# Kernel tuning notes

Hardware: AMD Instinct MI355X
Metric: run time of the kernel (lower is better)

Reference implementation:

```python
import jax, jax.numpy as jnp
import numpy as np

N, E, M = 4096, 65536, 16   # nodes, edges, channel multiplicity per degree
MID = 32                    # RadialFunc hidden width (SE3-Transformer default)
EPS = 1e-5                  # BatchNorm1d eps
DEGS = [0, 1]
PAIRS = [(0, 0), (0, 1), (1, 0), (1, 1)]  # (d_in, d_out)


def _bn_relu(x, g, b):
    # BatchNorm1d in training mode (biased batch stats over edges) + ReLU
    mu = x.mean(0, keepdims=True)
    var = ((x - mu) ** 2).mean(0, keepdims=True)
    return jax.nn.relu((x - mu) / jnp.sqrt(var + EPS) * g + b)


def _radial(feat, w1, b1, g1, be1, w2, b2, g2, be2, w3, b3, nf):
    # RadialFunc: Linear-BN-ReLU, Linear-BN-ReLU, Linear -> [E, nc_out, 1, nc_in, 1, nf]
    y = _bn_relu(feat @ w1 + b1, g1, be1)
    y = _bn_relu(y @ w2 + b2, g2, be2)
    y = y @ w3 + b3
    return y.reshape(-1, M, 1, M, 1, nf)


def _forward(h0, h1, r, basis00, basis01, basis10, basis11,
             rw1, rb1, rg1, rbe1, rw2, rb2, rg2, rbe2,
             w3_00, b3_00, w3_01, b3_01, w3_10, b3_10, w3_11, b3_11,
             Wself0, Wself1, edge_src, edge_dst):
    h = {0: h0, 1: h1}
    basis = {(0, 0): basis00, (0, 1): basis01, (1, 0): basis10, (1, 1): basis11}
    w3b3 = {(0, 0): (w3_00, b3_00), (0, 1): (w3_01, b3_01),
            (1, 0): (w3_10, b3_10), (1, 1): (w3_11, b3_11)}
    Wself = {0: Wself0, 1: Wself1}
    # PairwiseConv: per-edge kernel = sum_f R * basis  -> [E, M, 2do+1, M, 2di+1]
    kern = {}
    for p, (di, do) in enumerate(PAIRS):
        nf = 2 * min(di, do) + 1
        w3, b3 = w3b3[(di, do)]
        R = _radial(r, rw1[p], rb1[p], rg1[p], rbe1[p],
                    rw2[p], rb2[p], rg2[p], rbe2[p], w3, b3, nf)
        kern[(di, do)] = (R * basis[(di, do)]).sum(-1)
    cnt = jnp.maximum(
        jax.ops.segment_sum(jnp.ones((E,), h0.dtype), edge_dst, num_segments=N), 1.0)
    outs = []
    for do in DEGS:
        msg = jnp.zeros((E, M, 2 * do + 1), h0.dtype)
        for di in DEGS:
            # per-edge small matmul: kernel @ gathered source feature
            msg = msg + jnp.einsum('eopiq,eiq->eop', kern[(di, do)], h[di][edge_src])
        # self-interaction, flavor='skip': add W @ destination feature per edge
        msg = msg + jnp.einsum('mi,eip->emp', Wself[do][0], h[do][edge_dst])
        s = jax.ops.segment_sum(msg, edge_dst, num_segments=N)  # scatter-mean
        outs.append(s / cnt[:, None, None])
    return tuple(outs)


def setup_inputs() -> dict:
    key = jax.random.key(0)
    ks = jax.random.split(key, 20)
    nrm = lambda k, sh, s=1.0: jax.random.normal(k, sh, jnp.float32) * s
    return {
        'h0': nrm(ks[0], (N, M, 1)),
        'h1': nrm(ks[1], (N, M, 3)),
        'r': jax.random.uniform(ks[2], (E, 1), jnp.float32),
        'basis00': nrm(ks[3], (E, 1, 1, 1, 1, 1)),
        'basis01': nrm(ks[4], (E, 1, 3, 1, 1, 1)),
        'basis10': nrm(ks[5], (E, 1, 1, 1, 3, 1)),
        'basis11': nrm(ks[6], (E, 1, 3, 1, 3, 3)),
        'rw1': nrm(ks[7], (4, 1, MID)),
        'rb1': jnp.zeros((4, MID), jnp.float32),
        'rg1': jnp.ones((4, MID), jnp.float32),
        'rbe1': jnp.zeros((4, MID), jnp.float32),
        'rw2': nrm(ks[8], (4, MID, MID), 1.0 / np.sqrt(MID)),
        'rb2': jnp.zeros((4, MID), jnp.float32),
        'rg2': jnp.ones((4, MID), jnp.float32),
        'rbe2': jnp.zeros((4, MID), jnp.float32),
        'w3_00': nrm(ks[9], (MID, M * M), 1.0 / np.sqrt(MID)),
        'b3_00': jnp.zeros((M * M,), jnp.float32),
        'w3_01': nrm(ks[10], (MID, M * M), 1.0 / np.sqrt(MID)),
        'b3_01': jnp.zeros((M * M,), jnp.float32),
        'w3_10': nrm(ks[11], (MID, M * M), 1.0 / np.sqrt(MID)),
        'b3_10': jnp.zeros((M * M,), jnp.float32),
        'w3_11': nrm(ks[12], (MID, M * M * 3), 1.0 / np.sqrt(MID)),
        'b3_11': jnp.zeros((M * M * 3,), jnp.float32),
        'Wself0': nrm(ks[13], (1, M, M), 1.0 / np.sqrt(M)),
        'Wself1': nrm(ks[14], (1, M, M), 1.0 / np.sqrt(M)),
        'edge_src': jax.random.randint(ks[15], (E,), 0, N),
        'edge_dst': jax.random.randint(ks[16], (E,), 0, N),
    }


def reference(h0, h1, r, basis00, basis01, basis10, basis11,
              rw1, rb1, rg1, rbe1, rw2, rb2, rg2, rbe2,
              w3_00, b3_00, w3_01, b3_01, w3_10, b3_10, w3_11, b3_11,
              Wself0, Wself1, edge_src, edge_dst):
    return _forward(h0, h1, r, basis00, basis01, basis10, basis11,
                    rw1, rb1, rg1, rbe1, rw2, rb2, rg2, rbe2,
                    w3_00, b3_00, w3_01, b3_01, w3_10, b3_10, w3_11, b3_11,
                    Wself0, Wself1, edge_src, edge_dst)
```

## Files before the change

kernel.cpp:

```cpp
#include <hip/hip_runtime.h>

#define N_NODES 4096
#define N_EDGES 65536
#define MID 32
#define BN_EPS 1e-5f

#define WS_RSUM    0
#define WS_RSUMSQ  1
#define WS_ALPHA1  272
#define WS_BETA1   400
#define WS_A2      528
#define WS_S2      656
#define WS_W2T     16384
#define WS_GRAM    20480
#define WS_SUMY    24576
#define WS_MSG_F   262144
#define WS_U00     4456448
#define WS_U01     4521984
#define WS_V10     4587520
#define WS_W11     4784128
#define WS_DEG_I   1024
#define WS_CUR_I   5120
#define WS_OFFS_I  9216
#define WS_ELIST_I 65536
#define WSB_WA     524288
#define WSB_WB     557056
#define WSB_WC     573440

typedef short bf16x8 __attribute__((ext_vector_type(8)));
typedef float f32x4  __attribute__((ext_vector_type(4)));

__device__ __forceinline__ unsigned short f2bf(float x) {
    unsigned u = __float_as_uint(x);
    u += 0x7fffu + ((u >> 16) & 1u);
    return (unsigned short)(u >> 16);
}

__global__ void __launch_bounds__(256) k_pre(const float* __restrict__ rw2,
        const float* __restrict__ w300, const float* __restrict__ w301,
        const float* __restrict__ w310, const float* __restrict__ w311,
        const float* __restrict__ bw300, const float* __restrict__ bw301,
        const float* __restrict__ bw310, const float* __restrict__ bw311,
        const float* __restrict__ r, const int* __restrict__ edst,
        const float* __restrict__ h0, const float* __restrict__ h1,
        float* __restrict__ wsf) {
    if (blockIdx.x < 128) {
        int t = blockIdx.x * 256 + threadIdx.x;
        char* wsb = (char*)wsf;
        if (t < 4096) {
            int p = t >> 10, rem = t & 1023, c = rem >> 5, k = rem & 31;
            wsf[WS_W2T + t] = rw2[(p << 10) + (k << 5) + c];
        }
        if (t < 16384) {
            int col = t >> 5, k = t & 31;
            float v = (col < 256) ? w300[(k << 8) + col] : w310[(k << 8) + (col - 256)];
            ((unsigned short*)(wsb + WSB_WA))[t] = f2bf(v);
        }
        if (t < 8192) {
            int col = t >> 5, k = t & 31;
            ((unsigned short*)(wsb + WSB_WB))[t] = f2bf(w301[(k << 8) + col]);
        }
        if (t < 24576) {
            int col = t >> 5, k = t & 31;
            int f = col >> 8, rem = col & 255;
            ((unsigned short*)(wsb + WSB_WC))[t] = f2bf(w311[k * 768 + rem * 3 + f]);
        }
    } else if (blockIdx.x < 384) {
        int e = (blockIdx.x - 128) * 256 + threadIdx.x;
        float v = r[e];
        atomicAdd(((int*)wsf) + WS_DEG_I + edst[e], 1);
        float s = v, ss = v * v;
#pragma unroll
        for (int mk = 32; mk >= 1; mk >>= 1) {
            s  += __shfl_xor(s,  mk, 64);
            ss += __shfl_xor(ss, mk, 64);
        }
        __shared__ float ls[4], lss[4];
        int lane = threadIdx.x & 63, wv = threadIdx.x >> 6;
        if (lane == 0) { ls[wv] = s; lss[wv] = ss; }
        __syncthreads();
        if (threadIdx.x == 0) {
            atomicAdd(wsf + WS_RSUM,   ls[0] + ls[1] + ls[2] + ls[3]);
            atomicAdd(wsf + WS_RSUMSQ, lss[0] + lss[1] + lss[2] + lss[3]);
        }
    } else {
        int g = (blockIdx.x - 384) * 256 + threadIdx.x;
        int n = g >> 4, mo = g & 15;
        float s00 = 0.f, s01 = 0.f;
#pragma unroll
        for (int mi = 0; mi < 16; ++mi) {
            float hv = h0[n * 16 + mi];
            s00 += bw300[mo * 16 + mi] * hv;
            s01 += bw301[mo * 16 + mi] * hv;
        }
        wsf[WS_U00 + n * 16 + mo] = s00;
        wsf[WS_U01 + n * 16 + mo] = s01;
#pragma unroll
        for (int q = 0; q < 3; ++q) {
            float sv = 0.f;
#pragma unroll
            for (int mi = 0; mi < 16; ++mi)
                sv += bw310[mo * 16 + mi] * h1[n * 48 + mi * 3 + q];
            wsf[WS_V10 + n * 48 + q * 16 + mo] = sv;
        }
#pragma unroll 1
        for (int f = 0; f < 3; ++f)
#pragma unroll 1
            for (int q = 0; q < 3; ++q) {
                float sv = 0.f;
#pragma unroll
                for (int mi = 0; mi < 16; ++mi)
                    sv += bw311[(mo * 16 + mi) * 3 + f] * h1[n * 48 + mi * 3 + q];
                wsf[WS_W11 + n * 144 + (f * 3 + q) * 16 + mo] = sv;
            }
    }
}

__global__ void __launch_bounds__(512) k_gram(const float* __restrict__ r,
        const float* __restrict__ rw1, const float* __restrict__ rg1,
        const float* __restrict__ rbe1, float* __restrict__ wsf) {
    int t = threadIdx.x;
    int wv = t >> 6, lane = t & 63;
    int quad = lane >> 4, lq = lane & 15;
    int p  = __builtin_amdgcn_readfirstlane(wv & 3);
    int mt = __builtin_amdgcn_readfirstlane(wv >> 2);
    float mu_r  = wsf[WS_RSUM] * (1.f / N_EDGES);
    float var_r = wsf[WS_RSUMSQ] * (1.f / N_EDGES) - mu_r * mu_r;
    float al[2], be[2];
#pragma unroll
    for (int hh = 0; hh < 2; ++hh) {
        int ch = p * 32 + hh * 16 + lq;
        float w1 = rw1[ch];
        float a = w1 * rg1[ch] * rsqrtf(w1 * w1 * var_r + BN_EPS);
        al[hh] = a;
        be[hh] = rbe1[ch] - a * mu_r;
    }
    bf16x8 ones;
#pragma unroll
    for (int j = 0; j < 8; ++j) ones[j] = (short)0x3F80;
    f32x4 accG0 = {0.f, 0.f, 0.f, 0.f};
    f32x4 accG1 = {0.f, 0.f, 0.f, 0.f};
    f32x4 accS  = {0.f, 0.f, 0.f, 0.f};
    int ebase = blockIdx.x * 1024;
#pragma unroll 1
    for (int ks = 0; ks < 32; ++ks) {
        const float* rp = r + ebase + ks * 32 + quad * 8;
        float4 ra = *(const float4*)(rp);
        float4 rb = *(const float4*)(rp + 4);
        float rv[8] = {ra.x, ra.y, ra.z, ra.w, rb.x, rb.y, rb.z, rb.w};
        bf16x8 fr0, fr1;
#pragma unroll
        for (int j = 0; j < 8; ++j) {
            fr0[j] = (short)f2bf(fmaxf(0.f, al[0] * rv[j] + be[0]));
            fr1[j] = (short)f2bf(fmaxf(0.f, al[1] * rv[j] + be[1]));
        }
        bf16x8 fA = mt ? fr1 : fr0;
        accG0 = __builtin_amdgcn_mfma_f32_16x16x32_bf16(fA, fr0, accG0, 0, 0, 0);
        accG1 = __builtin_amdgcn_mfma_f32_16x16x32_bf16(fA, fr1, accG1, 0, 0, 0);
        accS  = __builtin_amdgcn_mfma_f32_16x16x32_bf16(fA, ones, accS,  0, 0, 0);
    }
    float* G = wsf + WS_GRAM + p * 1024;
#pragma unroll
    for (int reg = 0; reg < 4; ++reg) {
        int k1 = mt * 16 + quad * 4 + reg;
        atomicAdd(&G[k1 * 32 + lq],      accG0[reg]);
        atomicAdd(&G[k1 * 32 + 16 + lq], accG1[reg]);
    }
    if (lq == 0) {
#pragma unroll
        for (int reg = 0; reg < 4; ++reg)
            atomicAdd(wsf + WS_SUMY + p * 32 + mt * 16 + quad * 4 + reg, accS[reg]);
    }
}

__global__ void __launch_bounds__(1024) k_fs(const float* __restrict__ rw1,
        const float* __restrict__ rg1, const float* __restrict__ rbe1,
        const float* __restrict__ rg2, const float* __restrict__ rbe2,
        const float* __restrict__ rb2, float* __restrict__ wsf) {
    int t = threadIdx.x;
    if (t < 128) {
        float mu_r  = wsf[WS_RSUM] * (1.f / N_EDGES);
        float var_r = wsf[WS_RSUMSQ] * (1.f / N_EDGES) - mu_r * mu_r;
        float w1 = rw1[t];
        float al = w1 * rg1[t] * rsqrtf(w1 * w1 * var_r + BN_EPS);
        wsf[WS_ALPHA1 + t] = al;
        wsf[WS_BETA1  + t] = rbe1[t] - al * mu_r;
        int p = t >> 5, c = t & 31;
        const float* G = wsf + WS_GRAM + p * 1024;
        const float* w = wsf + WS_W2T + p * 1024 + c * 32;
        float invE = 1.f / N_EDGES;
        float s1 = 0.f;
#pragma unroll 1
        for (int k = 0; k < 32; ++k) s1 += w[k] * (wsf[WS_SUMY + p * 32 + k] * invE);
        float q = 0.f;
#pragma unroll 1
        for (int k1 = 0; k1 < 32; ++k1) {
            float a = 0.f;
#pragma unroll
            for (int k2 = 0; k2 < 32; ++k2) a += w[k2] * G[k1 * 32 + k2];
            q += w[k1] * a;
        }
        float var = q * invE - s1 * s1;
        float a2 = rg2[t] * rsqrtf(var + BN_EPS);
        wsf[WS_A2 + t] = a2;
        float mu2 = rb2[t] + s1;
        wsf[WS_S2 + t] = rbe2[t] - mu2 * a2;
    }
    __shared__ int sdata[1024];
    const int* deg = ((const int*)wsf) + WS_DEG_I;
    int* offs = ((int*)wsf) + WS_OFFS_I;
    int* cur  = ((int*)wsf) + WS_CUR_I;
    int v0 = deg[t * 4], v1 = deg[t * 4 + 1], v2 = deg[t * 4 + 2], v3 = deg[t * 4 + 3];
    sdata[t] = v0 + v1 + v2 + v3;
    __syncthreads();
    for (int off = 1; off < 1024; off <<= 1) {
        int x = sdata[t];
        int y = (t >= off) ? sdata[t - off] : 0;
        __syncthreads();
        sdata[t] = x + y;
        __syncthreads();
    }
    int excl = (t == 0) ? 0 : sdata[t - 1];
    int o0 = excl, o1 = excl + v0, o2 = o1 + v1, o3 = o2 + v2;
    offs[t * 4] = o0;     cur[t * 4] = o0;
    offs[t * 4 + 1] = o1; cur[t * 4 + 1] = o1;
    offs[t * 4 + 2] = o2; cur[t * 4 + 2] = o2;
    offs[t * 4 + 3] = o3; cur[t * 4 + 3] = o3;
    if (t == 1023) offs[4096] = sdata[1023];
}

__global__ void k_bucket(const int* __restrict__ edst, float* __restrict__ wsf) {
    int e = blockIdx.x * 256 + threadIdx.x;
    int d = edst[e];
    int* cur   = ((int*)wsf) + WS_CUR_I;
    int* elist = ((int*)wsf) + WS_ELIST_I;
    int pos = atomicAdd(&cur[d], 1);
    elist[pos] = e;
}

__global__ void __launch_bounds__(256) k_corr(const float* __restrict__ b00,
        const float* __restrict__ b01, const float* __restrict__ b10,
        const float* __restrict__ b11, const int* __restrict__ esrc,
        const float* __restrict__ wsf, float* __restrict__ msg) {
    int g = blockIdx.x * 256 + threadIdx.x;
    int e = g >> 2, quad = g & 3;
    int s = esrc[e];
    float4 u00q = *(const float4*)(wsf + WS_U00 + s * 16 + quad * 4);
    float b00v = b00[e];
    float m0[4];
#pragma unroll
    for (int rr = 0; rr < 4; ++rr) m0[rr] = b00v * ((const float*)&u00q)[rr];
#pragma unroll
    for (int q = 0; q < 3; ++q) {
        float4 vq = *(const float4*)(wsf + WS_V10 + s * 48 + q * 16 + quad * 4);
        float bq = b10[e * 3 + q];
#pragma unroll
        for (int rr = 0; rr < 4; ++rr) m0[rr] += bq * ((const float*)&vq)[rr];
    }
    {
        float4 w = {m0[0], m0[1], m0[2], m0[3]};
        *(float4*)(msg + (size_t)e * 64 + quad * 4) = w;
    }
    float4 u01q = *(const float4*)(wsf + WS_U01 + s * 16 + quad * 4);
    float bo0 = b01[e * 3 + 0], bo1 = b01[e * 3 + 1], bo2 = b01[e * 3 + 2];
    float m1[4][3];
#pragma unroll
    for (int rr = 0; rr < 4; ++rr) {
        float u = ((const float*)&u01q)[rr];
        m1[rr][0] = bo0 * u; m1[rr][1] = bo1 * u; m1[rr][2] = bo2 * u;
    }
#pragma unroll
    for (int f = 0; f < 3; ++f)
#pragma unroll
        for (int q = 0; q < 3; ++q) {
            float4 wq = *(const float4*)(wsf + WS_W11 + s * 144 + (f * 3 + q) * 16 + quad * 4);
#pragma unroll
            for (int o = 0; o < 3; ++o) {
                float bas = b11[e * 27 + o * 9 + q * 3 + f];
#pragma unroll
                for (int rr = 0; rr < 4; ++rr) m1[rr][o] += bas * ((const float*)&wq)[rr];
            }
        }
    float* base = msg + (size_t)e * 64 + 16 + quad * 12;
    float4 w0 = {m1[0][0], m1[0][1], m1[0][2], m1[1][0]};
    float4 w1 = {m1[1][1], m1[1][2], m1[2][0], m1[2][1]};
    float4 w2 = {m1[2][2], m1[3][0], m1[3][1], m1[3][2]};
    *(float4*)(base)     = w0;
    *(float4*)(base + 4) = w1;
    *(float4*)(base + 8) = w2;
}

__device__ __forceinline__ void y2_lds16(int p, int el, int c0, float rv,
                                         const float* __restrict__ wsf,
                                         const float* __restrict__ rb2, char* dst) {
    float y1[MID];
#pragma unroll
    for (int k = 0; k < MID; ++k)
        y1[k] = fmaxf(0.f, wsf[WS_ALPHA1 + p * 32 + k] * rv + wsf[WS_BETA1 + p * 32 + k]);
    unsigned short h[16];
#pragma unroll
    for (int cc = 0; cc < 16; ++cc) {
        int c = c0 + cc;
        float x = rb2[p * 32 + c];
#pragma unroll
        for (int k = 0; k < MID; ++k) x += y1[k] * wsf[WS_W2T + p * 1024 + c * 32 + k];
        h[cc] = f2bf(fmaxf(0.f, wsf[WS_A2 + p * 32 + c] * x + wsf[WS_S2 + p * 32 + c]));
    }
#pragma unroll
    for (int q = 0; q < 2; ++q) {
        int4 pk;
        pk.x = (int)h[q * 8 + 0] | ((int)h[q * 8 + 1] << 16);
        pk.y = (int)h[q * 8 + 2] | ((int)h[q * 8 + 3] << 16);
        pk.z = (int)h[q * 8 + 4] | ((int)h[q * 8 + 5] << 16);
        pk.w = (int)h[q * 8 + 6] | ((int)h[q * 8 + 7] << 16);
        *(int4*)(dst + el * 64 + c0 * 2 + q * 16) = pk;
    }
}

__global__ void __launch_bounds__(512, 2) k_msg(const float* __restrict__ r,
        const float* __restrict__ h0, const float* __restrict__ h1,
        const float* __restrict__ b00, const float* __restrict__ b01,
        const float* __restrict__ b10, const float* __restrict__ b11,
        const float* __restrict__ rb2,
        const int* __restrict__ esrc,
        const float* __restrict__ wsf, float* __restrict__ msg) {
    extern __shared__ char smem[];
    short* w3s = (short*)smem;
    const char* wsb = (const char*)wsf;
    int t = threadIdx.x;
    int wv = t >> 6, lane = t & 63;
    int quad = lane >> 4, lq = lane & 15;
    int eb = blockIdx.x << 8;

    {
        const float4* src = (const float4*)(wsb + WSB_WA);
        float4* dst = (float4*)smem;
#pragma unroll
        for (int i = 0; i < 4; ++i) dst[i * 512 + t] = src[i * 512 + t];
    }
    {
        int p = __builtin_amdgcn_readfirstlane((t >> 8) * 2);
        int el = t & 255;
        float rv = r[eb + el];
        char* dst = smem + 32768 + (t >> 8) * 16384;
        y2_lds16(p, el, 0, rv, wsf, rb2, dst);
        y2_lds16(p, el, 16, rv, wsf, rb2, dst);
    }
    __syncthreads();
#pragma unroll
    for (int g2 = 0; g2 < 2; ++g2) {
        int el = (wv * 2 + g2) * 16 + lq;
        int e = eb + el;
        int s = esrc[e];
        bf16x8 bf0 = *(const bf16x8*)(smem + 32768 + el * 64 + quad * 16);
        bf16x8 bf2 = *(const bf16x8*)(smem + 49152 + el * 64 + quad * 16);
        float4 h0q = *(const float4*)(h0 + s * 16 + quad * 4);
        float4 hv0 = *(const float4*)(h1 + s * 48 + quad * 12);
        float4 hv1 = *(const float4*)(h1 + s * 48 + quad * 12 + 4);
        float4 hv2 = *(const float4*)(h1 + s * 48 + quad * 12 + 8);
        float b00v = b00[e];
        float bq0 = b10[e * 3 + 0], bq1 = b10[e * 3 + 1], bq2 = b10[e * 3 + 2];
        float gq0 = bq0 * hv0.x + bq1 * hv0.y + bq2 * hv0.z;
        float gq1 = bq0 * hv0.w + bq1 * hv1.x + bq2 * hv1.y;
        float gq2 = bq0 * hv1.z + bq1 * hv1.w + bq2 * hv2.x;
        float gq3 = bq0 * hv2.y + bq1 * hv2.z + bq2 * hv2.w;
        float4 a0v = *(const float4*)(msg + (size_t)e * 64 + quad * 4);
        float a0[4] = {a0v.x, a0v.y, a0v.z, a0v.w};
#pragma unroll
        for (int m = 0; m < 16; ++m) {
            bf16x8 af = *(const bf16x8*)(w3s + (m * 16 + lq) * 32 + quad * 8);
            f32x4 dd = __builtin_amdgcn_mfma_f32_16x16x32_bf16(af, bf0, (f32x4){0.f,0.f,0.f,0.f}, 0, 0, 0);
            float partial = dd[0] * h0q.x + dd[1] * h0q.y + dd[2] * h0q.z + dd[3] * h0q.w;
            partial += __shfl_xor(partial, 16);
            partial += __shfl_xor(partial, 32);
            a0[m & 3] += (quad == (m >> 2)) ? b00v * partial : 0.f;
        }
#pragma unroll
        for (int m = 0; m < 16; ++m) {
            bf16x8 af = *(const bf16x8*)(w3s + ((256 + m * 16 + lq) << 5) + quad * 8);
            f32x4 dd = __builtin_amdgcn_mfma_f32_16x16x32_bf16(af, bf2, (f32x4){0.f,0.f,0.f,0.f}, 0, 0, 0);
            float partial = dd[0] * gq0 + dd[1] * gq1 + dd[2] * gq2 + dd[3] * gq3;
            partial += __shfl_xor(partial, 16);
            partial += __shfl_xor(partial, 32);
            a0[m & 3] += (quad == (m >> 2)) ? partial : 0.f;
        }
        float4 w = {a0[0], a0[1], a0[2], a0[3]};
        *(float4*)(msg + (size_t)e * 64 + quad * 4) = w;
    }
    __syncthreads();

    {
        const float4* src = (const float4*)(wsb + WSB_WB);
        float4* dst = (float4*)smem;
#pragma unroll
        for (int i = 0; i < 2; ++i) dst[i * 512 + t] = src[i * 512 + t];
    }
    {
        int el = t & 255, c0 = (t >> 8) * 16;
        y2_lds16(1, el, c0, r[eb + el], wsf, rb2, smem + 16384);
    }
    __syncthreads();
#pragma unroll
    for (int g2 = 0; g2 < 2; ++g2) {
        int el = (wv * 2 + g2) * 16 + lq;
        int e = eb + el;
        int s = esrc[e];
        bf16x8 bf1 = *(const bf16x8*)(smem + 16384 + el * 64 + quad * 16);
        float4 h0q = *(const float4*)(h0 + s * 16 + quad * 4);
        float d1[4] = {0.f, 0.f, 0.f, 0.f};
#pragma unroll
        for (int m = 0; m < 16; ++m) {
            bf16x8 af = *(const bf16x8*)(w3s + (m * 16 + lq) * 32 + quad * 8);
            f32x4 dd = __builtin_amdgcn_mfma_f32_16x16x32_bf16(af, bf1, (f32x4){0.f,0.f,0.f,0.f}, 0, 0, 0);
            float partial = dd[0] * h0q.x + dd[1] * h0q.y + dd[2] * h0q.z + dd[3] * h0q.w;
            partial += __shfl_xor(partial, 16);
            partial += __shfl_xor(partial, 32);
            d1[m & 3] += (quad == (m >> 2)) ? partial : 0.f;
        }
        float bo0 = b01[e * 3 + 0], bo1 = b01[e * 3 + 1], bo2 = b01[e * 3 + 2];
        float* base = msg + (size_t)e * 64 + 16 + quad * 12;
        float4 r0 = *(const float4*)(base);
        float4 r1 = *(const float4*)(base + 4);
        float4 r2 = *(const float4*)(base + 8);
        float4 w0 = {r0.x + bo0 * d1[0], r0.y + bo1 * d1[0], r0.z + bo2 * d1[0], r0.w + bo0 * d1[1]};
        float4 w1 = {r1.x + bo1 * d1[1], r1.y + bo2 * d1[1], r1.z + bo0 * d1[2], r1.w + bo1 * d1[2]};
        float4 w2 = {r2.x + bo2 * d1[2], r2.y + bo0 * d1[3], r2.z + bo1 * d1[3], r2.w + bo2 * d1[3]};
        *(float4*)(base)     = w0;
        *(float4*)(base + 4) = w1;
        *(float4*)(base + 8) = w2;
    }
    __syncthreads();

    {
        const float4* src = (const float4*)(wsb + WSB_WC);
        float4* dst = (float4*)smem;
#pragma unroll
        for (int i = 0; i < 6; ++i) dst[i * 512 + t] = src[i * 512 + t];
    }
    {
        int el = t & 255, c0 = (t >> 8) * 16;
        y2_lds16(3, el, c0, r[eb + el], wsf, rb2, smem + 49152);
    }
    __syncthreads();
#pragma unroll
    for (int g2 = 0; g2 < 2; ++g2) {
        int el = (wv * 2 + g2) * 16 + lq;
        int e = eb + el;
        int s = esrc[e];
        bf16x8 bf3 = *(const bf16x8*)(smem + 49152 + el * 64 + quad * 16);
        float4 hv0 = *(const float4*)(h1 + s * 48 + quad * 12);
        float4 hv1 = *(const float4*)(h1 + s * 48 + quad * 12 + 4);
        float4 hv2 = *(const float4*)(h1 + s * 48 + quad * 12 + 8);
        float h1v[4][3] = {{hv0.x, hv0.y, hv0.z}, {hv0.w, hv1.x, hv1.y},
                           {hv1.z, hv1.w, hv2.x}, {hv2.y, hv2.z, hv2.w}};
        float m1[4][3];
#pragma unroll
        for (int rr = 0; rr < 4; ++rr)
#pragma unroll
            for (int o = 0; o < 3; ++o) m1[rr][o] = 0.f;
#pragma unroll
        for (int f = 0; f < 3; ++f) {
            float Tf[4][3];
#pragma unroll
            for (int o = 0; o < 3; ++o) {
                float bv0 = b11[e * 27 + o * 9 + 0 + f];
                float bv1 = b11[e * 27 + o * 9 + 3 + f];
                float bv2 = b11[e * 27 + o * 9 + 6 + f];
#pragma unroll
                for (int rr = 0; rr < 4; ++rr)
                    Tf[rr][o] = h1v[rr][0] * bv0 + h1v[rr][1] * bv1 + h1v[rr][2] * bv2;
            }
#pragma unroll
            for (int m = 0; m < 16; ++m) {
                int colb = f * 256 + m * 16 + lq;
                bf16x8 af = *(const bf16x8*)(w3s + colb * 32 + quad * 8);
                f32x4 dd = __builtin_amdgcn_mfma_f32_16x16x32_bf16(af, bf3, (f32x4){0.f,0.f,0.f,0.f}, 0, 0, 0);
#pragma unroll
                for (int o = 0; o < 3; ++o) {
                    float po = dd[0] * Tf[0][o] + dd[1] * Tf[1][o] + dd[2] * Tf[2][o] + dd[3] * Tf[3][o];
                    po += __shfl_xor(po, 16);
                    po += __shfl_xor(po, 32);
                    m1[m & 3][o] += (quad == (m >> 2)) ? po : 0.f;
                }
            }
        }
        float* base = msg + (size_t)e * 64 + 16 + quad * 12;
        float4 r0 = *(const float4*)(base);
        float4 r1 = *(const float4*)(base + 4);
        float4 r2 = *(const float4*)(base + 8);
        float4 w0 = {m1[0][0] + r0.x, m1[0][1] + r0.y, m1[0][2] + r0.z, m1[1][0] + r0.w};
        float4 w1 = {m1[1][1] + r1.x, m1[1][2] + r1.y, m1[2][0] + r1.z, m1[2][1] + r1.w};
        float4 w2 = {m1[2][2] + r2.x, m1[3][0] + r2.y, m1[3][1] + r2.z, m1[3][2] + r2.w};
        *(float4*)(base)     = w0;
        *(float4*)(base + 4) = w1;
        *(float4*)(base + 8) = w2;
    }
}

__global__ void __launch_bounds__(256) k_gather(const float* __restrict__ h0,
        const float* __restrict__ h1, const float* __restrict__ Wself0,
        const float* __restrict__ Wself1, const float* __restrict__ wsf,
        float* __restrict__ out) {
    int wv = threadIdx.x >> 6, lane = threadIdx.x & 63;
    int n = blockIdx.x * 4 + wv;
    const int* offs  = ((const int*)wsf) + WS_OFFS_I;
    const int* elist = ((const int*)wsf) + WS_ELIST_I;
    const float* msg = wsf + WS_MSG_F;
    int start = offs[n], end = offs[n + 1];
    int deg = end - start;
    float acc = 0.f;
    for (int j0 = 0; j0 < deg; j0 += 64) {
        int cnt = min(64, deg - j0);
        int eidv = (j0 + lane < deg) ? elist[start + j0 + lane] : 0;
        for (int jj = 0; jj < cnt; ++jj) {
            int eid = __shfl(eidv, jj);
            acc += msg[(size_t)eid * 64 + lane];
        }
    }
    float self = 0.f;
    if (lane < 16) {
        int m = lane;
#pragma unroll
        for (int i = 0; i < 16; ++i) self += Wself0[m * 16 + i] * h0[n * 16 + i];
    } else {
        int idx = lane - 16; int m = idx / 3, o = idx % 3;
#pragma unroll
        for (int i = 0; i < 16; ++i) self += Wself1[m * 16 + i] * h1[n * 48 + i * 3 + o];
    }
    float c = (float)(deg > 0 ? deg : 1);
    float res = acc / c + (deg > 0 ? self : 0.f);
    if (lane < 16) out[n * 16 + lane] = res;
    else           out[65536 + n * 48 + (lane - 16)] = res;
}

extern "C" void kernel_launch(void* const* d_in, const int* in_sizes, int n_in,
                              void* d_out, int out_size, void* d_ws, size_t ws_size,
                              hipStream_t stream) {
    const float* h0   = (const float*)d_in[0];
    const float* h1   = (const float*)d_in[1];
    const float* r    = (const float*)d_in[2];
    const float* b00  = (const float*)d_in[3];
    const float* b01  = (const float*)d_in[4];
    const float* b10  = (const float*)d_in[5];
    const float* b11  = (const float*)d_in[6];
    const float* rw1  = (const float*)d_in[7];
    const float* rg1  = (const float*)d_in[9];
    const float* rbe1 = (const float*)d_in[10];
    const float* rw2  = (const float*)d_in[11];
    const float* rb2  = (const float*)d_in[12];
    const float* rg2  = (const float*)d_in[13];
    const float* rbe2 = (const float*)d_in[14];
    const float* w300 = (const float*)d_in[15];
    const float* bw300= (const float*)d_in[16];
    const float* w301 = (const float*)d_in[17];
    const float* bw301= (const float*)d_in[18];
    const float* w310 = (const float*)d_in[19];
    const float* bw310= (const float*)d_in[20];
    const float* w311 = (const float*)d_in[21];
    const float* bw311= (const float*)d_in[22];
    const float* Wself0 = (const float*)d_in[23];
    const float* Wself1 = (const float*)d_in[24];
    const int* esrc = (const int*)d_in[25];
    const int* edst = (const int*)d_in[26];
    float* out = (float*)d_out;
    float* wsf = (float*)d_ws;
    float* msg = wsf + WS_MSG_F;

    static bool attr_set = false;
    if (!attr_set) {
        hipFuncSetAttribute((const void*)k_msg,
                            hipFuncAttributeMaxDynamicSharedMemorySize, 65536);
        attr_set = true;
    }

    hipMemsetAsync(d_ws, 0, 20480, stream);
    hipMemsetAsync((char*)d_ws + 81920, 0, 16896, stream);

    k_pre<<<640, 256, 0, stream>>>(rw2, w300, w301, w310, w311,
                                   bw300, bw301, bw310, bw311, r, edst, h0, h1, wsf);
    k_gram<<<64, 512, 0, stream>>>(r, rw1, rg1, rbe1, wsf);
    k_fs<<<1, 1024, 0, stream>>>(rw1, rg1, rbe1, rg2, rbe2, rb2, wsf);
    k_bucket<<<256, 256, 0, stream>>>(edst, wsf);
    k_corr<<<1024, 256, 0, stream>>>(b00, b01, b10, b11, esrc, wsf, msg);
    k_msg<<<256, 512, 65536, stream>>>(r, h0, h1, b00, b01, b10, b11, rb2,
                                       esrc, wsf, msg);
    k_gather<<<1024, 256, 0, stream>>>(h0, h1, Wself0, Wself1, wsf, out);
}
```

Measured before the change: 265.7 us.

## Fuse bias-correction pass into message kernel, halve edges per block, unroll gather

Removes the separate k_corr kernel and computes its U00/V10/U01/W11 correction terms directly inside k_msg, so the message buffer is no longer written and then read back for every edge. k_msg now handles 128 edges per block over 512 blocks with smaller shared memory, and each wave processes one 16-edge group instead of two. k_gram is split across twice as many blocks, the workspace is rearranged so a single memset covers it, and the gather loop is unrolled by four to keep more loads in flight. The trade-off is more per-thread arithmetic in k_msg and half the threads sitting idle during some y2 staging phases.

New measurement: 307.9 us. 15.9% more time.

```diff
diff --git a/kernel.cpp b/kernel.cpp
--- a/kernel.cpp
+++ b/kernel.cpp
@@ -11,17 +11,17 @@
 #define WS_BETA1   400
 #define WS_A2      528
 #define WS_S2      656
-#define WS_W2T     16384
-#define WS_GRAM    20480
-#define WS_SUMY    24576
+#define WS_GRAM    5120
+#define WS_SUMY    9216
+#define WS_W2T     17664
 #define WS_MSG_F   262144
 #define WS_U00     4456448
 #define WS_U01     4521984
 #define WS_V10     4587520
 #define WS_W11     4784128
 #define WS_DEG_I   1024
-#define WS_CUR_I   5120
-#define WS_OFFS_I  9216
+#define WS_CUR_I   9344
+#define WS_OFFS_I  13440
 #define WS_ELIST_I 65536
 #define WSB_WA     524288
 #define WSB_WB     557056
@@ -141,9 +141,9 @@
     f32x4 accG0 = {0.f, 0.f, 0.f, 0.f};
     f32x4 accG1 = {0.f, 0.f, 0.f, 0.f};
     f32x4 accS  = {0.f, 0.f, 0.f, 0.f};
-    int ebase = blockIdx.x * 1024;
+    int ebase = blockIdx.x * 512;
 #pragma unroll 1
-    for (int ks = 0; ks < 32; ++ks) {
+    for (int ks = 0; ks < 16; ++ks) {
         const float* rp = r + ebase + ks * 32 + quad * 8;
         float4 ra = *(const float4*)(rp);
         float4 rb = *(const float4*)(rp + 4);
@@ -238,58 +238,6 @@
     elist[pos] = e;
 }
 
-__global__ void __launch_bounds__(256) k_corr(const float* __restrict__ b00,
-        const float* __restrict__ b01, const float* __restrict__ b10,
-        const float* __restrict__ b11, const int* __restrict__ esrc,
-        const float* __restrict__ wsf, float* __restrict__ msg) {
-    int g = blockIdx.x * 256 + threadIdx.x;
-    int e = g >> 2, quad = g & 3;
-    int s = esrc[e];
-    float4 u00q = *(const float4*)(wsf + WS_U00 + s * 16 + quad * 4);
-    float b00v = b00[e];
-    float m0[4];
-#pragma unroll
-    for (int rr = 0; rr < 4; ++rr) m0[rr] = b00v * ((const float*)&u00q)[rr];
-#pragma unroll
-    for (int q = 0; q < 3; ++q) {
-        float4 vq = *(const float4*)(wsf + WS_V10 + s * 48 + q * 16 + quad * 4);
-        float bq = b10[e * 3 + q];
-#pragma unroll
-        for (int rr = 0; rr < 4; ++rr) m0[rr] += bq * ((const float*)&vq)[rr];
-    }
-    {
-        float4 w = {m0[0], m0[1], m0[2], m0[3]};
-        *(float4*)(msg + (size_t)e * 64 + quad * 4) = w;
-    }
-    float4 u01q = *(const float4*)(wsf + WS_U01 + s * 16 + quad * 4);
-    float bo0 = b01[e * 3 + 0], bo1 = b01[e * 3 + 1], bo2 = b01[e * 3 + 2];
-    float m1[4][3];
-#pragma unroll
-    for (int rr = 0; rr < 4; ++rr) {
-        float u = ((const float*)&u01q)[rr];
-        m1[rr][0] = bo0 * u; m1[rr][1] = bo1 * u; m1[rr][2] = bo2 * u;
-    }
-#pragma unroll
-    for (int f = 0; f < 3; ++f)
-#pragma unroll
-        for (int q = 0; q < 3; ++q) {
-            float4 wq = *(const float4*)(wsf + WS_W11 + s * 144 + (f * 3 + q) * 16 + quad * 4);
-#pragma unroll
-            for (int o = 0; o < 3; ++o) {
-                float bas = b11[e * 27 + o * 9 + q * 3 + f];
-#pragma unroll
-                for (int rr = 0; rr < 4; ++rr) m1[rr][o] += bas * ((const float*)&wq)[rr];
-            }
-        }
-    float* base = msg + (size_t)e * 64 + 16 + quad * 12;
-    float4 w0 = {m1[0][0], m1[0][1], m1[0][2], m1[1][0]};
-    float4 w1 = {m1[1][1], m1[1][2], m1[2][0], m1[2][1]};
-    float4 w2 = {m1[2][2], m1[3][0], m1[3][1], m1[3][2]};
-    *(float4*)(base)     = w0;
-    *(float4*)(base + 4) = w1;
-    *(float4*)(base + 8) = w2;
-}
-
 __device__ __forceinline__ void y2_lds16(int p, int el, int c0, float rv,
                                          const float* __restrict__ wsf,
                                          const float* __restrict__ rb2, char* dst) {
@@ -330,7 +278,9 @@
     int t = threadIdx.x;
     int wv = t >> 6, lane = t & 63;
     int quad = lane >> 4, lq = lane & 15;
-    int eb = blockIdx.x << 8;
+    int eb = blockIdx.x << 7;
+    int el = wv * 16 + lq;
+    int e = eb + el;
 
     {
         const float4* src = (const float4*)(wsb + WSB_WA);
@@ -339,21 +289,17 @@
         for (int i = 0; i < 4; ++i) dst[i * 512 + t] = src[i * 512 + t];
     }
     {
-        int p = __builtin_amdgcn_readfirstlane((t >> 8) * 2);
-        int el = t & 255;
-        float rv = r[eb + el];
-        char* dst = smem + 32768 + (t >> 8) * 16384;
-        y2_lds16(p, el, 0, rv, wsf, rb2, dst);
-        y2_lds16(p, el, 16, rv, wsf, rb2, dst);
+        int g = t >> 7;
+        int p = __builtin_amdgcn_readfirstlane((g >> 1) * 2);
+        int c0 = (g & 1) * 16;
+        int el2 = t & 127;
+        y2_lds16(p, el2, c0, r[eb + el2], wsf, rb2, smem + 32768 + (g >> 1) * 8192);
     }
     __syncthreads();
-#pragma unroll
-    for (int g2 = 0; g2 < 2; ++g2) {
-        int el = (wv * 2 + g2) * 16 + lq;
-        int e = eb + el;
+    {
         int s = esrc[e];
         bf16x8 bf0 = *(const bf16x8*)(smem + 32768 + el * 64 + quad * 16);
-        bf16x8 bf2 = *(const bf16x8*)(smem + 49152 + el * 64 + quad * 16);
+        bf16x8 bf2 = *(const bf16x8*)(smem + 40960 + el * 64 + quad * 16);
         float4 h0q = *(const float4*)(h0 + s * 16 + quad * 4);
         float4 hv0 = *(const float4*)(h1 + s * 48 + quad * 12);
         float4 hv1 = *(const float4*)(h1 + s * 48 + quad * 12 + 4);
@@ -364,8 +310,14 @@
         float gq1 = bq0 * hv0.w + bq1 * hv1.x + bq2 * hv1.y;
         float gq2 = bq0 * hv1.z + bq1 * hv1.w + bq2 * hv2.x;
         float gq3 = bq0 * hv2.y + bq1 * hv2.z + bq2 * hv2.w;
-        float4 a0v = *(const float4*)(msg + (size_t)e * 64 + quad * 4);
-        float a0[4] = {a0v.x, a0v.y, a0v.z, a0v.w};
+        float4 u00q = *(const float4*)(wsf + WS_U00 + s * 16 + quad * 4);
+        float a0[4] = {b00v * u00q.x, b00v * u00q.y, b00v * u00q.z, b00v * u00q.w};
+#pragma unroll
+        for (int q = 0; q < 3; ++q) {
+            float4 vq = *(const float4*)(wsf + WS_V10 + s * 48 + q * 16 + quad * 4);
+            float bq = (q == 0) ? bq0 : ((q == 1) ? bq1 : bq2);
+            a0[0] += bq * vq.x; a0[1] += bq * vq.y; a0[2] += bq * vq.z; a0[3] += bq * vq.w;
+        }
 #pragma unroll
         for (int m = 0; m < 16; ++m) {
             bf16x8 af = *(const bf16x8*)(w3s + (m * 16 + lq) * 32 + quad * 8);
@@ -395,19 +347,17 @@
 #pragma unroll
         for (int i = 0; i < 2; ++i) dst[i * 512 + t] = src[i * 512 + t];
     }
-    {
-        int el = t & 255, c0 = (t >> 8) * 16;
-        y2_lds16(1, el, c0, r[eb + el], wsf, rb2, smem + 16384);
+    if (t < 256) {
+        int el2 = t & 127, c0 = (t >> 7) * 16;
+        y2_lds16(1, el2, c0, r[eb + el2], wsf, rb2, smem + 16384);
     }
     __syncthreads();
-#pragma unroll
-    for (int g2 = 0; g2 < 2; ++g2) {
-        int el = (wv * 2 + g2) * 16 + lq;
-        int e = eb + el;
+    {
         int s = esrc[e];
         bf16x8 bf1 = *(const bf16x8*)(smem + 16384 + el * 64 + quad * 16);
         float4 h0q = *(const float4*)(h0 + s * 16 + quad * 4);
-        float d1[4] = {0.f, 0.f, 0.f, 0.f};
+        float4 u01q = *(const float4*)(wsf + WS_U01 + s * 16 + quad * 4);
+        float d1[4] = {u01q.x, u01q.y, u01q.z, u01q.w};
 #pragma unroll
         for (int m = 0; m < 16; ++m) {
             bf16x8 af = *(const bf16x8*)(w3s + (m * 16 + lq) * 32 + quad * 8);
@@ -419,12 +369,9 @@
         }
         float bo0 = b01[e * 3 + 0], bo1 = b01[e * 3 + 1], bo2 = b01[e * 3 + 2];
         float* base = msg + (size_t)e * 64 + 16 + quad * 12;
-        float4 r0 = *(const float4*)(base);
-        float4 r1 = *(const float4*)(base + 4);
-        float4 r2 = *(const float4*)(base + 8);
-        float4 w0 = {r0.x + bo0 * d1[0], r0.y + bo1 * d1[0], r0.z + bo2 * d1[0], r0.w + bo0 * d1[1]};
-        float4 w1 = {r1.x + bo1 * d1[1], r1.y + bo2 * d1[1], r1.z + bo0 * d1[2], r1.w + bo1 * d1[2]};
-        float4 w2 = {r2.x + bo2 * d1[2], r2.y + bo0 * d1[3], r2.z + bo1 * d1[3], r2.w + bo2 * d1[3]};
+        float4 w0 = {bo0 * d1[0], bo1 * d1[0], bo2 * d1[0], bo0 * d1[1]};
+        float4 w1 = {bo1 * d1[1], bo2 * d1[1], bo0 * d1[2], bo1 * d1[2]};
+        float4 w2 = {bo2 * d1[2], bo0 * d1[3], bo1 * d1[3], bo2 * d1[3]};
         *(float4*)(base)     = w0;
         *(float4*)(base + 4) = w1;
         *(float4*)(base + 8) = w2;
@@ -437,15 +384,12 @@
 #pragma unroll
         for (int i = 0; i < 6; ++i) dst[i * 512 + t] = src[i * 512 + t];
     }
-    {
-        int el = t & 255, c0 = (t >> 8) * 16;
-        y2_lds16(3, el, c0, r[eb + el], wsf, rb2, smem + 49152);
+    if (t < 256) {
+        int el2 = t & 127, c0 = (t >> 7) * 16;
+        y2_lds16(3, el2, c0, r[eb + el2], wsf, rb2, smem + 49152);
     }
     __syncthreads();
-#pragma unroll
-    for (int g2 = 0; g2 < 2; ++g2) {
-        int el = (wv * 2 + g2) * 16 + lq;
-        int e = eb + el;
+    {
         int s = esrc[e];
         bf16x8 bf3 = *(const bf16x8*)(smem + 49152 + el * 64 + quad * 16);
         float4 hv0 = *(const float4*)(h1 + s * 48 + quad * 12);
@@ -460,6 +404,9 @@
             for (int o = 0; o < 3; ++o) m1[rr][o] = 0.f;
 #pragma unroll
         for (int f = 0; f < 3; ++f) {
+            float4 wq0 = *(const float4*)(wsf + WS_W11 + s * 144 + (f * 3 + 0) * 16 + quad * 4);
+            float4 wq1 = *(const float4*)(wsf + WS_W11 + s * 144 + (f * 3 + 1) * 16 + quad * 4);
+            float4 wq2 = *(const float4*)(wsf + WS_W11 + s * 144 + (f * 3 + 2) * 16 + quad * 4);
             float Tf[4][3];
 #pragma unroll
             for (int o = 0; o < 3; ++o) {
@@ -469,6 +416,10 @@
 #pragma unroll
                 for (int rr = 0; rr < 4; ++rr)
                     Tf[rr][o] = h1v[rr][0] * bv0 + h1v[rr][1] * bv1 + h1v[rr][2] * bv2;
+                m1[0][o] += bv0 * wq0.x + bv1 * wq1.x + bv2 * wq2.x;
+                m1[1][o] += bv0 * wq0.y + bv1 * wq1.y + bv2 * wq2.y;
+                m1[2][o] += bv0 * wq0.z + bv1 * wq1.z + bv2 * wq2.z;
+                m1[3][o] += bv0 * wq0.w + bv1 * wq1.w + bv2 * wq2.w;
             }
 #pragma unroll
             for (int m = 0; m < 16; ++m) {
@@ -512,7 +463,17 @@
     for (int j0 = 0; j0 < deg; j0 += 64) {
         int cnt = min(64, deg - j0);
         int eidv = (j0 + lane < deg) ? elist[start + j0 + lane] : 0;
-        for (int jj = 0; jj < cnt; ++jj) {
+        int jj = 0;
+        for (; jj + 3 < cnt; jj += 4) {
+            int e0 = __shfl(eidv, jj), e1 = __shfl(eidv, jj + 1);
+            int e2 = __shfl(eidv, jj + 2), e3 = __shfl(eidv, jj + 3);
+            float v0 = msg[(size_t)e0 * 64 + lane];
+            float v1 = msg[(size_t)e1 * 64 + lane];
+            float v2 = msg[(size_t)e2 * 64 + lane];
+            float v3 = msg[(size_t)e3 * 64 + lane];
+            acc += (v0 + v1) + (v2 + v3);
+        }
+        for (; jj < cnt; ++jj) {
             int eid = __shfl(eidv, jj);
             acc += msg[(size_t)eid * 64 + lane];
         }
@@ -569,20 +530,18 @@
     static bool attr_set = false;
     if (!attr_set) {
         hipFuncSetAttribute((const void*)k_msg,
-                            hipFuncAttributeMaxDynamicSharedMemorySize, 65536);
+                            hipFuncAttributeMaxDynamicSharedMemorySize, 57344);
         attr_set = true;
     }
 
-    hipMemsetAsync(d_ws, 0, 20480, stream);
-    hipMemsetAsync((char*)d_ws + 81920, 0, 16896, stream);
+    hipMemsetAsync(d_ws, 0, 37376, stream);
 
     k_pre<<<640, 256, 0, stream>>>(rw2, w300, w301, w310, w311,
                                    bw300, bw301, bw310, bw311, r, edst, h0, h1, wsf);
-    k_gram<<<64, 512, 0, stream>>>(r, rw1, rg1, rbe1, wsf);
+    k_gram<<<128, 512, 0, stream>>>(r, rw1, rg1, rbe1, wsf);
     k_fs<<<1, 1024, 0, stream>>>(rw1, rg1, rbe1, rg2, rbe2, rb2, wsf);
     k_bucket<<<256, 256, 0, stream>>>(edst, wsf);
-    k_corr<<<1024, 256, 0, stream>>>(b00, b01, b10, b11, esrc, wsf, msg);
-    k_msg<<<256, 512, 65536, stream>>>(r, h0, h1, b00, b01, b10, b11, rb2,
+    k_msg<<<512, 512, 57344, stream>>>(r, h0, h1, b00, b01, b10, b11, rb2,
                                        esrc, wsf, msg);
     k_gather<<<1024, 256, 0, stream>>>(h0, h1, Wself0, Wself1, wsf, out);
 }
```
